# Kernel tuning notes

Measured on AMD Instinct MI355X. Metric: run time of the kernel, lower is better.

Reference implementation:

```python
import jax, jax.numpy as jnp
import numpy as np

B, T, V, E, H, O = 64, 2048, 50000, 256, 256, 16

def setup_inputs() -> dict:
    key = jax.random.key(0)
    ks = jax.random.split(key, 10)
    s_rnn = 1.0 / np.sqrt(H)
    s_fc1 = 1.0 / np.sqrt(H)
    s_fc2 = 1.0 / np.sqrt(H // 2)
    return {
        "x": jax.random.randint(ks[0], (B, T), 0, V, dtype=jnp.int32),
        "emb": jax.random.normal(ks[1], (V, E), dtype=jnp.float32),
        "W_ih": jax.random.uniform(ks[2], (H, E), jnp.float32, -s_rnn, s_rnn),
        "W_hh": jax.random.uniform(ks[3], (H, H), jnp.float32, -s_rnn, s_rnn),
        "b_ih": jax.random.uniform(ks[4], (H,), jnp.float32, -s_rnn, s_rnn),
        "b_hh": jax.random.uniform(ks[5], (H,), jnp.float32, -s_rnn, s_rnn),
        "fc1_w": jax.random.uniform(ks[6], (H // 2, H), jnp.float32, -s_fc1, s_fc1),
        "fc1_b": jax.random.uniform(ks[7], (H // 2,), jnp.float32, -s_fc1, s_fc1),
        "fc2_w": jax.random.uniform(ks[8], (O, H // 2), jnp.float32, -s_fc2, s_fc2),
        "fc2_b": jax.random.uniform(ks[9], (O,), jnp.float32, -s_fc2, s_fc2),
    }

def reference(x, emb, W_ih, W_hh, b_ih, b_hh, fc1_w, fc1_b, fc2_w, fc2_b):
    # Embedding lookup: [B, T, E]
    e = emb[x]
    # Precompute input-to-hidden projection for all timesteps in one big GEMM
    xh = jnp.einsum("bte,he->bth", e, W_ih) + b_ih + b_hh  # [B, T, H]
    h0 = jnp.zeros((x.shape[0], W_hh.shape[0]), dtype=e.dtype)

    def step(h, xt):  # h: [B, H], xt: [B, H]
        h = jnp.tanh(xt + h @ W_hh.T)
        return h, None

    h_last, _ = jax.lax.scan(step, h0, jnp.swapaxes(xh, 0, 1))  # final hidden [B, H]
    # Dropout is identity at inference. MLP head: fc1 -> relu -> fc2
    hid = jax.nn.relu(h_last @ fc1_w.T + fc1_b)
    return hid @ fc2_w.T + fc2_b  # [B, O]
```

## Files before the change

kernel.cpp:

```cpp
#include <hip/hip_runtime.h>
#include <hip/hip_bf16.h>


#define B_  64
#define T_  2048
#define E_  256
#define H_  256
#define O_  16
#define H2_ 128
#define CH  4
#define HP  272

typedef _Float16 f16x2 __attribute__((ext_vector_type(2)));
typedef _Float16 f16x4 __attribute__((ext_vector_type(4)));
typedef _Float16 f16x8 __attribute__((ext_vector_type(8)));
typedef float    f32x4 __attribute__((ext_vector_type(4)));

#define LDS_BARRIER() asm volatile("s_waitcnt lgkmcnt(0)\n\ts_barrier" ::: "memory")

__device__ __forceinline__ float tanh_fast(float x) {
  const float e = __expf(2.0f * x);
  return fmaf(-2.0f, __builtin_amdgcn_rcpf(e + 1.0f), 1.0f);
}

__device__ __forceinline__ f32x4 cvt4(f16x4 v) {
  return (f32x4){(float)v[0], (float)v[1], (float)v[2], (float)v[3]};
}

__global__ __launch_bounds__(256) void k0_cvt(
    const float* __restrict__ W_ih, const float* __restrict__ W_hh,
    _Float16* __restrict__ Wih16, _Float16* __restrict__ Whh16) {
  const int i = (blockIdx.x * 256 + threadIdx.x) * 4;
  if (i < H_ * E_) {
    float4 a = *(const float4*)&W_ih[i];
    float4 b = *(const float4*)&W_hh[i];
    f16x4 ah, bh;
    ah[0]=(_Float16)a.x; ah[1]=(_Float16)a.y; ah[2]=(_Float16)a.z; ah[3]=(_Float16)a.w;
    bh[0]=(_Float16)b.x; bh[1]=(_Float16)b.y; bh[2]=(_Float16)b.z; bh[3]=(_Float16)b.w;
    *(f16x4*)&Wih16[i] = ah;
    *(f16x4*)&Whh16[i] = bh;
  }
}

__global__ __launch_bounds__(256) void k1_xh(
    const int* __restrict__ x, const float* __restrict__ emb,
    const _Float16* __restrict__ Wih16, const float* __restrict__ b_ih,
    const float* __restrict__ b_hh, _Float16* __restrict__ xh) {
  __shared__ _Float16 A16[64][264];
  const int tid  = threadIdx.x;
  const int w    = tid >> 6;
  const int lane = tid & 63;
  const int nl   = lane & 15;
  const int koff = (lane >> 4) << 3;
  const long r0  = (long)blockIdx.x * 64;

  {
    const int c4 = lane << 2;
#pragma unroll
    for (int it = 0; it < 16; ++it) {
      const int row = (it << 2) + w;
      const long tok = x[r0 + row];
      const float4 v = *(const float4*)&emb[tok * E_ + c4];
      f16x4 hv;
      hv[0] = (_Float16)v.x; hv[1] = (_Float16)v.y;
      hv[2] = (_Float16)v.z; hv[3] = (_Float16)v.w;
      *(f16x4*)&A16[row][c4] = hv;
    }
  }

  f16x8 bfr[4][8];
#pragma unroll
  for (int nt = 0; nt < 4; ++nt) {
    const int n = (w << 6) + (nt << 4) + nl;
#pragma unroll
    for (int kt = 0; kt < 8; ++kt)
      bfr[nt][kt] = *(const f16x8*)&Wih16[n * E_ + (kt << 5) + koff];
  }
  __syncthreads();

  f32x4 acc[4][4];
#pragma unroll
  for (int mt = 0; mt < 4; ++mt)
#pragma unroll
    for (int nt = 0; nt < 4; ++nt) acc[mt][nt] = (f32x4){};

#pragma unroll
  for (int mt = 0; mt < 4; ++mt) {
#pragma unroll
    for (int kt = 0; kt < 8; ++kt) {
      const f16x8 a = *(const f16x8*)&A16[(mt << 4) + nl][(kt << 5) + koff];
#pragma unroll
      for (int nt = 0; nt < 4; ++nt)
        acc[mt][nt] = __builtin_amdgcn_mfma_f32_16x16x32_f16(a, bfr[nt][kt], acc[mt][nt], 0, 0, 0);
    }
  }
  __syncthreads();

  {
    const int rsub = (lane >> 4) << 2;
#pragma unroll
    for (int nt = 0; nt < 4; ++nt) {
      const int n = (w << 6) + (nt << 4) + nl;
      const float bias = b_ih[n] + b_hh[n];
#pragma unroll
      for (int mt = 0; mt < 4; ++mt)
#pragma unroll
        for (int j = 0; j < 4; ++j)
          A16[(mt << 4) + rsub + j][n] = (_Float16)(acc[mt][nt][j] + bias);
    }
  }
  __syncthreads();

  {
#pragma unroll
    for (int i = 0; i < 8; ++i) {
      const int row = (w << 4) + (i << 1) + (lane >> 5);
      const int col = (lane & 31) << 3;
      *(f16x8*)&xh[(r0 + row) * H_ + col] = *(const f16x8*)&A16[row][col];
    }
  }
}

__global__ __launch_bounds__(512, 2) void k2_rnn(
    const _Float16* __restrict__ xh, const _Float16* __restrict__ Whh16,
    const float* __restrict__ fc1_w, const float* __restrict__ fc1_b,
    const float* __restrict__ fc2_w, const float* __restrict__ fc2_b,
    float* __restrict__ out) {
  __shared__ _Float16 h16[2][CH][HP];
  __shared__ float    hid_s[CH][H2_ + 4];

  const int tid   = threadIdx.x;
  const int w     = tid >> 6;
  const int lane  = tid & 63;
  const int nl    = lane & 15;
  const int quad  = lane >> 4;
  const int cc    = nl & (CH - 1);
  const int g     = nl >> 2;
  const int mtsel = g & 1;
  const int jp    = g >> 1;
  const int koff  = quad << 3;
  const int rwb   = (w << 5) + (quad << 2);
  const int c0    = blockIdx.x * CH;

  f16x8 afr[2][8];
#pragma unroll
  for (int mt = 0; mt < 2; ++mt) {
    const int r = (w << 5) + (mt << 4) + nl;
#pragma unroll
    for (int kt = 0; kt < 8; ++kt)
      afr[mt][kt] = *(const f16x8*)&Whh16[r * H_ + (kt << 5) + koff];
  }

  const _Float16* xb = xh + (size_t)(c0 + cc) * T_ * H_ + rwb;
  f16x4 xq0[4], xq1[4], xn0[4], xn1[4];
#pragma unroll
  for (int s = 0; s < 4; ++s) {
    xq0[s] = *(const f16x4*)&xb[(size_t)s * H_];
    xq1[s] = *(const f16x4*)&xb[(size_t)s * H_ + 16];
  }
#pragma unroll
  for (int s = 0; s < 4; ++s) {
    xn0[s] = *(const f16x4*)&xb[(size_t)(4 + s) * H_];
    xn1[s] = *(const f16x4*)&xb[(size_t)(4 + s) * H_ + 16];
  }

  if (tid < 128) *(f16x8*)&h16[0][tid >> 5][(tid & 31) << 3] = (f16x8){};
  __syncthreads();

#define BODY(P, S)                                                             \
  {                                                                            \
    f16x8 bfr[8];                                                              \
    _Pragma("unroll")                                                          \
    for (int i = 0; i < 8; ++i)                                                \
      bfr[i] = *(const f16x8*)&h16[P][cc][(i << 5) + koff];                    \
    f32x4 ca0 = __builtin_amdgcn_mfma_f32_16x16x32_f16(afr[0][0], bfr[0], cvt4(xq0[S]), 0, 0, 0); \
    f32x4 ca1 = __builtin_amdgcn_mfma_f32_16x16x32_f16(afr[1][0], bfr[0], cvt4(xq1[S]), 0, 0, 0); \
    f32x4 cb0 = __builtin_amdgcn_mfma_f32_16x16x32_f16(afr[0][4], bfr[4], (f32x4){}, 0, 0, 0); \
    f32x4 cb1 = __builtin_amdgcn_mfma_f32_16x16x32_f16(afr[1][4], bfr[4], (f32x4){}, 0, 0, 0); \
    _Pragma("unroll")                                                          \
    for (int i = 1; i < 4; ++i) {                                              \
      ca0 = __builtin_amdgcn_mfma_f32_16x16x32_f16(afr[0][i], bfr[i], ca0, 0, 0, 0);         \
      ca1 = __builtin_amdgcn_mfma_f32_16x16x32_f16(afr[1][i], bfr[i], ca1, 0, 0, 0);         \
      cb0 = __builtin_amdgcn_mfma_f32_16x16x32_f16(afr[0][4 + i], bfr[4 + i], cb0, 0, 0, 0); \
      cb1 = __builtin_amdgcn_mfma_f32_16x16x32_f16(afr[1][4 + i], bfr[4 + i], cb1, 0, 0, 0); \
    }                                                                          \
    const f32x4 s0 = ca0 + cb0;                                                \
    const f32x4 s1 = ca1 + cb1;                                                \
    const f32x4 sm = mtsel ? s1 : s0;                                          \
    const float u0 = jp ? sm[2] : sm[0];                                       \
    const float u1 = jp ? sm[3] : sm[1];                                       \
    f16x2 o;                                                                   \
    o[0] = (_Float16)tanh_fast(u0);                                            \
    o[1] = (_Float16)tanh_fast(u1);                                            \
    *(f16x2*)&h16[P ^ 1][cc][rwb + (mtsel << 4) + (jp << 1)] = o;              \
    LDS_BARRIER();                                                             \
  }

  for (int tt = 0; tt < T_; tt += 4) {
    BODY(0, 0)
    BODY(1, 1)
    BODY(0, 2)
    BODY(1, 3)
#pragma unroll
    for (int s = 0; s < 4; ++s) { xq0[s] = xn0[s]; xq1[s] = xn1[s]; }
    const int tn = tt + 8;
#pragma unroll
    for (int s = 0; s < 4; ++s) {
      const size_t ti = (size_t)((tn + s) & (T_ - 1)) * H_;
      xn0[s] = *(const f16x4*)&xb[ti];
      xn1[s] = *(const f16x4*)&xb[ti + 16];
    }
  }
#undef BODY

  __syncthreads();

  {
    const int pc = tid >> 7;
    const int o_ = tid & 127;
    float s = fc1_b[o_];
#pragma unroll 8
    for (int k = 0; k < H_; ++k) s += fc1_w[o_ * H_ + k] * (float)h16[0][pc][k];
    hid_s[pc][o_] = fmaxf(s, 0.f);
  }
  __syncthreads();
  if (tid < CH * O_) {
    const int c = tid >> 4, o_ = tid & 15;
    float s = fc2_b[o_];
#pragma unroll 8
    for (int k = 0; k < H2_; ++k) s += fc2_w[o_ * H2_ + k] * hid_s[c][k];
    out[(size_t)(c0 + c) * O_ + o_] = s;
  }
}

extern "C" void kernel_launch(void* const* d_in, const int* in_sizes, int n_in,
                              void* d_out, int out_size, void* d_ws, size_t ws_size,
                              hipStream_t stream) {
  const int*   x     = (const int*)d_in[0];
  const float* emb   = (const float*)d_in[1];
  const float* W_ih  = (const float*)d_in[2];
  const float* W_hh  = (const float*)d_in[3];
  const float* b_ih  = (const float*)d_in[4];
  const float* b_hh  = (const float*)d_in[5];
  const float* fc1_w = (const float*)d_in[6];
  const float* fc1_b = (const float*)d_in[7];
  const float* fc2_w = (const float*)d_in[8];
  const float* fc2_b = (const float*)d_in[9];
  float* outp = (float*)d_out;

  _Float16* xh16  = (_Float16*)d_ws;
  _Float16* Wih16 = xh16 + (size_t)B_ * T_ * H_;
  _Float16* Whh16 = Wih16 + (size_t)H_ * E_;

  k0_cvt<<<dim3(H_ * E_ / 1024), dim3(256), 0, stream>>>(W_ih, W_hh, Wih16, Whh16);
  k1_xh<<<dim3(B_ * T_ / 64), dim3(256), 0, stream>>>(x, emb, Wih16, b_ih, b_hh, xh16);
  k2_rnn<<<dim3(B_ / CH), dim3(512), 0, stream>>>(xh16, Whh16, fc1_w, fc1_b, fc2_w, fc2_b, outp);
}
```

Before: 1.417 ms.

## Split RNN recurrence across 16 waves, one 16-row tile per wave

The recurrent kernel now launches 1024 threads per block instead of 512, so each wave computes one 16-row tile of W_hh·h instead of two. This halves the serial MFMA chain per wave per timestep. W_hh is staged through shared memory before being loaded into register fragments. Each lane now writes a single fp16 hidden value instead of a pair. The exchange adds more waves to every per-step barrier and 128KB of LDS for the staged weights, which may lengthen barrier latency.

```diff
diff --git a/kernel.cpp b/kernel.cpp
--- a/kernel.cpp
+++ b/kernel.cpp
@@ -121,11 +121,13 @@
   }
 }
 
-__global__ __launch_bounds__(512, 2) void k2_rnn(
+__global__ __attribute__((amdgpu_flat_work_group_size(1024, 1024)))
+__attribute__((amdgpu_waves_per_eu(4, 4))) void k2_rnn(
     const _Float16* __restrict__ xh, const _Float16* __restrict__ Whh16,
     const float* __restrict__ fc1_w, const float* __restrict__ fc1_b,
     const float* __restrict__ fc2_w, const float* __restrict__ fc2_b,
     float* __restrict__ out) {
+  __shared__ _Float16 whh_s[H_ * H_];
   __shared__ _Float16 h16[2][CH][HP];
   __shared__ float    hid_s[CH][H2_ + 4];
 
@@ -136,36 +138,34 @@
   const int quad  = lane >> 4;
   const int cc    = nl & (CH - 1);
   const int g     = nl >> 2;
-  const int mtsel = g & 1;
-  const int jp    = g >> 1;
   const int koff  = quad << 3;
-  const int rwb   = (w << 5) + (quad << 2);
+  const int wrow  = (w << 4) + (quad << 2);
   const int c0    = blockIdx.x * CH;
 
-  f16x8 afr[2][8];
-#pragma unroll
-  for (int mt = 0; mt < 2; ++mt) {
-    const int r = (w << 5) + (mt << 4) + nl;
+  {
+#pragma unroll
+    for (int c = 0; c < 8; ++c) {
+      const int idx = ((c << 10) + tid) << 3;
+      *(f16x8*)&whh_s[idx] = *(const f16x8*)&Whh16[idx];
+    }
+  }
+  if (tid < 128) *(f16x8*)&h16[0][tid >> 5][(tid & 31) << 3] = (f16x8){};
+  __syncthreads();
+
+  f16x8 afr[8];
+  {
+    const int r = (w << 4) + nl;
 #pragma unroll
     for (int kt = 0; kt < 8; ++kt)
-      afr[mt][kt] = *(const f16x8*)&Whh16[r * H_ + (kt << 5) + koff];
-  }
-
-  const _Float16* xb = xh + (size_t)(c0 + cc) * T_ * H_ + rwb;
-  f16x4 xq0[4], xq1[4], xn0[4], xn1[4];
-#pragma unroll
-  for (int s = 0; s < 4; ++s) {
-    xq0[s] = *(const f16x4*)&xb[(size_t)s * H_];
-    xq1[s] = *(const f16x4*)&xb[(size_t)s * H_ + 16];
-  }
-#pragma unroll
-  for (int s = 0; s < 4; ++s) {
-    xn0[s] = *(const f16x4*)&xb[(size_t)(4 + s) * H_];
-    xn1[s] = *(const f16x4*)&xb[(size_t)(4 + s) * H_ + 16];
-  }
-
-  if (tid < 128) *(f16x8*)&h16[0][tid >> 5][(tid & 31) << 3] = (f16x8){};
-  __syncthreads();
+      afr[kt] = *(const f16x8*)&whh_s[r * H_ + (kt << 5) + koff];
+  }
+
+  const _Float16* xb = xh + (size_t)(c0 + cc) * T_ * H_ + wrow;
+  f16x4 xq[4], xn[4];
+#pragma unroll
+  for (int s = 0; s < 4; ++s) xq[s] = *(const f16x4*)&xb[(size_t)s * H_];
+#pragma unroll
+  for (int s = 0; s < 4; ++s) xn[s] = *(const f16x4*)&xb[(size_t)(4 + s) * H_];
 
 #define BODY(P, S)                                                             \
   {                                                                            \
@@ -173,26 +173,18 @@
     _Pragma("unroll")                                                          \
     for (int i = 0; i < 8; ++i)                                                \
       bfr[i] = *(const f16x8*)&h16[P][cc][(i << 5) + koff];                    \
-    f32x4 ca0 = __builtin_amdgcn_mfma_f32_16x16x32_f16(afr[0][0], bfr[0], cvt4(xq0[S]), 0, 0, 0); \
-    f32x4 ca1 = __builtin_amdgcn_mfma_f32_16x16x32_f16(afr[1][0], bfr[0], cvt4(xq1[S]), 0, 0, 0); \
-    f32x4 cb0 = __builtin_amdgcn_mfma_f32_16x16x32_f16(afr[0][4], bfr[4], (f32x4){}, 0, 0, 0); \
-    f32x4 cb1 = __builtin_amdgcn_mfma_f32_16x16x32_f16(afr[1][4], bfr[4], (f32x4){}, 0, 0, 0); \
+    f32x4 ca = __builtin_amdgcn_mfma_f32_16x16x32_f16(afr[0], bfr[0], cvt4(xq[S]), 0, 0, 0); \
+    f32x4 cb = __builtin_amdgcn_mfma_f32_16x16x32_f16(afr[4], bfr[4], (f32x4){}, 0, 0, 0);   \
     _Pragma("unroll")                                                          \
     for (int i = 1; i < 4; ++i) {                                              \
-      ca0 = __builtin_amdgcn_mfma_f32_16x16x32_f16(afr[0][i], bfr[i], ca0, 0, 0, 0);         \
-      ca1 = __builtin_amdgcn_mfma_f32_16x16x32_f16(afr[1][i], bfr[i], ca1, 0, 0, 0);         \
-      cb0 = __builtin_amdgcn_mfma_f32_16x16x32_f16(afr[0][4 + i], bfr[4 + i], cb0, 0, 0, 0); \
-      cb1 = __builtin_amdgcn_mfma_f32_16x16x32_f16(afr[1][4 + i], bfr[4 + i], cb1, 0, 0, 0); \
+      ca = __builtin_amdgcn_mfma_f32_16x16x32_f16(afr[i], bfr[i], ca, 0, 0, 0);              \
+      cb = __builtin_amdgcn_mfma_f32_16x16x32_f16(afr[4 + i], bfr[4 + i], cb, 0, 0, 0);      \
     }                                                                          \
-    const f32x4 s0 = ca0 + cb0;                                                \
-    const f32x4 s1 = ca1 + cb1;                                                \
-    const f32x4 sm = mtsel ? s1 : s0;                                          \
-    const float u0 = jp ? sm[2] : sm[0];                                       \
-    const float u1 = jp ? sm[3] : sm[1];                                       \
-    f16x2 o;                                                                   \
-    o[0] = (_Float16)tanh_fast(u0);                                            \
-    o[1] = (_Float16)tanh_fast(u1);                                            \
-    *(f16x2*)&h16[P ^ 1][cc][rwb + (mtsel << 4) + (jp << 1)] = o;              \
+    const f32x4 s4 = ca + cb;                                                  \
+    const float u01 = (g & 1) ? s4[1] : s4[0];                                 \
+    const float u23 = (g & 1) ? s4[3] : s4[2];                                 \
+    const float u   = (g & 2) ? u23 : u01;                                     \
+    h16[P ^ 1][cc][wrow + g] = (_Float16)tanh_fast(u);                         \
     LDS_BARRIER();                                                             \
   }
 
@@ -202,20 +194,19 @@
     BODY(0, 2)
     BODY(1, 3)
 #pragma unroll
-    for (int s = 0; s < 4; ++s) { xq0[s] = xn0[s]; xq1[s] = xn1[s]; }
+    for (int s = 0; s < 4; ++s) xq[s] = xn[s];
     const int tn = tt + 8;
 #pragma unroll
     for (int s = 0; s < 4; ++s) {
       const size_t ti = (size_t)((tn + s) & (T_ - 1)) * H_;
-      xn0[s] = *(const f16x4*)&xb[ti];
-      xn1[s] = *(const f16x4*)&xb[ti + 16];
+      xn[s] = *(const f16x4*)&xb[ti];
     }
   }
 #undef BODY
 
   __syncthreads();
 
-  {
+  if (tid < 512) {
     const int pc = tid >> 7;
     const int o_ = tid & 127;
     float s = fc1_b[o_];
@@ -254,5 +245,5 @@
 
   k0_cvt<<<dim3(H_ * E_ / 1024), dim3(256), 0, stream>>>(W_ih, W_hh, Wih16, Whh16);
   k1_xh<<<dim3(B_ * T_ / 64), dim3(256), 0, stream>>>(x, emb, Wih16, b_ih, b_hh, xh16);
-  k2_rnn<<<dim3(B_ / CH), dim3(512), 0, stream>>>(xh16, Whh16, fc1_w, fc1_b, fc2_w, fc2_b, outp);
-}
+  k2_rnn<<<dim3(B_ / CH), dim3(1024), 0, stream>>>(xh16, Whh16, fc1_w, fc1_b, fc2_w, fc2_b, outp);
+}
```

New measurement: 1.294 ms. -8.7%, faster.
